# Kernel optimization log

Measured on AMD Instinct MI355X. Metric: run time of the kernel, lower is better.

## Reference

```python
import jax, jax.numpy as jnp
import numpy as np

N, F_IN, HID, HEADS, NEA, E, G = 50000, 32, 64, 2, 2, 800000, 50
SLOPE = 0.2  # leaky_relu negative_slope


def setup_inputs() -> dict:
    key = jax.random.key(0)
    ks = jax.random.split(key, 24)
    x = jax.random.normal(ks[0], (N, F_IN), jnp.float32)
    src = jax.random.randint(ks[1], (E,), 0, N, jnp.int32)
    off = jax.random.randint(ks[2], (E,), 1, N, jnp.int32)
    dst = ((src + off) % N).astype(jnp.int32)  # guaranteed no self loops
    edge_index = jnp.stack([src, dst])
    edge_attr = jax.random.uniform(ks[3], (E, NEA), jnp.float32, 0.5, 3.0)  # distances (reciprocal taken in fwd)
    batch = (jnp.arange(N) // (N // G)).astype(jnp.int32)
    interface_pos = jnp.arange(0, N, 5, dtype=jnp.int32)  # 200 interface nodes/graph

    def glorot(k, shape, fan_in, fan_out):
        s = jnp.sqrt(6.0 / (fan_in + fan_out))
        return jax.random.uniform(k, shape, jnp.float32, -s, s)

    HC = HEADS * HID
    W0 = glorot(ks[4], (F_IN, HC), F_IN, HC)
    attl0 = glorot(ks[5], (HEADS, HID), HID, HID)
    attr0 = glorot(ks[6], (HEADS, HID), HID, HID)
    W12 = glorot(ks[7], (2, HID, HC), HID, HC)
    attl12 = glorot(ks[8], (2, HEADS, HID), HID, HID)
    attr12 = glorot(ks[9], (2, HEADS, HID), HID, HID)
    eW = glorot(ks[10], (3, NEA, HC), NEA, HC)
    eb = jnp.zeros((3, HC), jnp.float32)
    bconv = jnp.zeros((3, HID), jnp.float32)
    gate_w = glorot(ks[11], (HID, 1), HID, 1)
    gate_b = jnp.zeros((1,), jnp.float32)
    lin1_w = glorot(ks[12], (4 * HID, 2 * HID), 4 * HID, 2 * HID)
    lin1_b = jnp.zeros((2 * HID,), jnp.float32)
    lin2_w = glorot(ks[13], (2 * HID, 1), 2 * HID, 1)
    lin2_b = jnp.zeros((1,), jnp.float32)
    return dict(x=x, edge_index=edge_index, edge_attr=edge_attr, batch=batch,
                interface_pos=interface_pos, graph_num=G,
                W0=W0, attl0=attl0, attr0=attr0, W12=W12, attl12=attl12, attr12=attr12,
                eW=eW, eb=eb, bconv=bconv, gate_w=gate_w, gate_b=gate_b,
                lin1_w=lin1_w, lin1_b=lin1_b, lin2_w=lin2_w, lin2_b=lin2_b)


def segment_softmax(e, seg, n):
    m = jax.ops.segment_max(e, seg, num_segments=n)
    ex = jnp.exp(e - m[seg])
    d = jax.ops.segment_sum(ex, seg, num_segments=n)
    return ex / (d[seg] + 1e-16)


def gate_conv(h, W, att_l, att_r, eW, eb, b, src, dst, ea):
    # GATEConv, concat=False, dropout in eval mode (identity)
    n = h.shape[0]
    H, C = att_l.shape
    xl = (h @ W).reshape(n, H, C)                      # lin_l == lin_r
    al = (xl * att_l).sum(-1)                          # [N,H]
    ar = (xl * att_r).sum(-1)
    e = jax.nn.leaky_relu(al[src] + ar[dst], SLOPE)    # [E+N,H]
    alpha = segment_softmax(e, dst, n)
    ee = (ea @ eW + eb).reshape(-1, H, C)              # edge embeddings
    msg = (xl[src] + ee) * alpha[..., None]
    out = jax.ops.segment_sum(msg, dst, num_segments=n)
    return out.mean(1) + b                             # mean over heads + bias


def reference(x, edge_index, edge_attr, batch, interface_pos, graph_num,
              W0, attl0, attr0, W12, attl12, attr12, eW, eb, bconv,
              gate_w, gate_b, lin1_w, lin1_b, lin2_w, lin2_b):
    n = x.shape[0]
    ar_n = jnp.arange(n, dtype=edge_index.dtype)
    src = jnp.concatenate([edge_index[0], ar_n])       # add self loops
    dst = jnp.concatenate([edge_index[1], ar_n])
    ea = jnp.concatenate([1.0 / edge_attr,
                          jnp.zeros((n, edge_attr.shape[1]), edge_attr.dtype)], 0)

    h = jnp.tanh(gate_conv(x, W0, attl0, attr0, eW[0], eb[0], bconv[0], src, dst, ea))
    xmax = h
    for l in range(2):  # num_layers - 1 structurally distinct weight slices
        h = jnp.tanh(gate_conv(h, W12[l], attl12[l], attr12[l],
                               eW[l + 1], eb[l + 1], bconv[l + 1], src, dst, ea))
        xmax = jnp.maximum(xmax, h)                    # JumpingKnowledge('max')

    xi = xmax[interface_pos]                           # [Ni, hidden]
    bi = batch[interface_pos]
    add = jax.ops.segment_sum(xi, bi, num_segments=graph_num)
    cnt = jax.ops.segment_sum(jnp.ones((xi.shape[0],), xi.dtype), bi, num_segments=graph_num)
    mean = add / jnp.maximum(cnt, 1.0)[:, None]
    gate = (xi @ gate_w + gate_b)[:, 0]                # global self-attention gate
    a = segment_softmax(gate, bi, graph_num)
    attp = jax.ops.segment_sum(a[:, None] * xi, bi, num_segments=graph_num)
    mx = jax.ops.segment_max(xi, bi, num_segments=graph_num)
    pooled = jnp.concatenate([add, mean, attp, mx], -1)  # [G, 4*hidden]
    z = jnp.tanh(pooled @ lin1_w + lin1_b)             # dropout eval = identity
    return z @ lin2_w + lin2_b                         # [G, 1]
```

## Files before the change

### kernel.cpp

```cpp
#include <hip/hip_runtime.h>
#include <hip/hip_bf16.h>
#include <hip/hip_fp16.h>
#include <math.h>

#define N_NODES 50000
#define FIN     32
#define HID     64
#define HC      128
#define NE      800000
#define NET     850000
#define NI      10000
#define NG      50
#define NPG     1000
#define NIPG    200
#define DMAX    64

#define EB512   ((NET + 511) / 512)
#define LBLK    (N_NODES / 16)

typedef _Float16 half8 __attribute__((ext_vector_type(8)));
typedef float float4v __attribute__((ext_vector_type(4)));

__device__ __forceinline__ float lrelu(float x) { return fmaxf(x, 0.2f * x); }

__device__ __forceinline__ float rlf(float v, int l) {
  return __int_as_float(__builtin_amdgcn_readlane(__float_as_int(v), l));
}
__device__ __forceinline__ int rli(int v, int l) {
  return __builtin_amdgcn_readlane(v, l);
}

template <int F>
__device__ __forceinline__ void lin8(
    int n0, const float* __restrict__ W,
    const float* __restrict__ attl, const float* __restrict__ attr,
    __half2* __restrict__ xl2h, float* __restrict__ al, float* __restrict__ ar,
    const _Float16* hA, _Float16* hC, float* redl, float* redr) {
  const int w = threadIdx.x >> 6, lane = threadIdx.x & 63;
  const int m = lane & 15, q = lane >> 4;

  half8 a0, a1;
#pragma unroll
  for (int j = 0; j < 8; j++) a0[j] = hA[m * F + q * 8 + j];
  if constexpr (F == 64) {
#pragma unroll
    for (int j = 0; j < 8; j++) a1[j] = hA[m * F + 32 + q * 8 + j];
  }

  const int colg = w * 16 + m;
  half8 b0;
#pragma unroll
  for (int j = 0; j < 8; j++) b0[j] = (_Float16)W[(q * 8 + j) * HC + colg];
  float4v z = {0.f, 0.f, 0.f, 0.f};
  float4v acc = __builtin_amdgcn_mfma_f32_16x16x32_f16(a0, b0, z, 0, 0, 0);
  if constexpr (F == 64) {
    half8 b1;
#pragma unroll
    for (int j = 0; j < 8; j++) b1[j] = (_Float16)W[(32 + q * 8 + j) * HC + colg];
    acc = __builtin_amdgcn_mfma_f32_16x16x32_f16(a1, b1, acc, 0, 0, 0);
  }
  const float atl = attl[colg], atr = attr[colg];
  float pl[4], pr[4];
#pragma unroll
  for (int reg = 0; reg < 4; reg++) {
    float val = acc[reg];
    hC[(q * 4 + reg) * 128 + colg] = (_Float16)val;
    pl[reg] = val * atl;
    pr[reg] = val * atr;
  }
#pragma unroll
  for (int off = 1; off < 16; off <<= 1) {
#pragma unroll
    for (int reg = 0; reg < 4; reg++) {
      pl[reg] += __shfl_xor(pl[reg], off, 64);
      pr[reg] += __shfl_xor(pr[reg], off, 64);
    }
  }
  if (m == 0) {
#pragma unroll
    for (int reg = 0; reg < 4; reg++) {
      redl[(q * 4 + reg) * 8 + w] = pl[reg];
      redr[(q * 4 + reg) * 8 + w] = pr[reg];
    }
  }
  __syncthreads();
  if (threadIdx.x < 32) {
    int node = threadIdx.x >> 1, head = threadIdx.x & 1;
    float sl = 0.f, sr = 0.f;
#pragma unroll
    for (int k = 0; k < 4; k++) {
      sl += redl[node * 8 + head * 4 + k];
      sr += redr[node * 8 + head * 4 + k];
    }
    al[(n0 + node) * 2 + head] = sl;
    ar[(n0 + node) * 2 + head] = sr;
  }
  for (int i = threadIdx.x; i < 16 * 64; i += 512) {
    int node = i >> 6, cc = i & 63;
    xl2h[(size_t)(n0 + node) * HID + cc] =
        __halves2half2(hC[node * 128 + cc], hC[node * 128 + 64 + cc]);
  }
}

__device__ __forceinline__ void agg_wave(
    int n0, const __half2* __restrict__ xl, const float* __restrict__ alp,
    const float2* __restrict__ ar2,
    const int* __restrict__ degarr, const int2* __restrict__ erec,
    const float* __restrict__ eW2, const float* __restrict__ eb1,
    const float* __restrict__ bconv1, float& outA, float& outB) {
  const int gid0 = n0 + ((threadIdx.x >> 6) << 1);
  const int lane = threadIdx.x & 63;
  const int l32 = lane & 31;
  const int half = lane >> 5;
  const int lane4 = lane << 2;
  const int gidH = gid0 + half;
  const int o0H = gidH * DMAX;
  const int degH = min(degarr[gidH], DMAX);
  const float2 arvH = ar2[gidH];
  const char* xbase = (const char*)xl;
  const char* albase = (const char*)alp;

  const int degA = rli(degH, 0);
  const int degB = rli(degH, 32);
  const int degmax = max(degA, degB);

  float aA0 = 0.f, aA1 = 0.f, bA0 = 0.f, bA1 = 0.f;
  float aB0 = 0.f, aB1 = 0.f, bB0 = 0.f, bB1 = 0.f;
  float ld0 = 0.f, ld1 = 0.f, lex0 = 0.f, ley0 = 0.f, lex1 = 0.f, ley1 = 0.f;

  for (int base = 0; base < degmax; base += 32) {
    int j = base + l32;
    int soff = 0; float p0 = 0.f, p1 = 0.f;
    if (j < degH) {
      int2 r = erec[o0H + j];
      soff = r.x;
      float2 eaf = __half22float2(*(__half2*)&r.y);
      float2 alv = *(const float2*)(albase + (soff >> 5));
      p0 = __expf(lrelu(alv.x + arvH.x));
      p1 = __expf(lrelu(alv.y + arvH.y));
      ld0 += p0; ld1 += p1;
      lex0 += p0 * eaf.x; ley0 += p0 * eaf.y;
      lex1 += p1 * eaf.x; ley1 += p1 * eaf.y;
    }
    int lenA = min(32, degA - base); lenA = max(lenA, 0);
    int lenB = min(32, degB - base); lenB = max(lenB, 0);
    int lenA4 = (lenA + 3) & ~3;
    int lenB4 = (lenB + 3) & ~3;
    int len = max(lenA4, lenB4);
    for (int j2 = 0; j2 < len; j2 += 4) {
      if (j2 < lenA4) {
        float2 x0 = __half22float2(*(const __half2*)(xbase + rli(soff, j2)     + lane4));
        float2 x1 = __half22float2(*(const __half2*)(xbase + rli(soff, j2 + 1) + lane4));
        float2 x2 = __half22float2(*(const __half2*)(xbase + rli(soff, j2 + 2) + lane4));
        float2 x3 = __half22float2(*(const __half2*)(xbase + rli(soff, j2 + 3) + lane4));
        aA0 += rlf(p0, j2)     * x0.x; aA1 += rlf(p1, j2)     * x0.y;
        bA0 += rlf(p0, j2 + 1) * x1.x; bA1 += rlf(p1, j2 + 1) * x1.y;
        aA0 += rlf(p0, j2 + 2) * x2.x; aA1 += rlf(p1, j2 + 2) * x2.y;
        bA0 += rlf(p0, j2 + 3) * x3.x; bA1 += rlf(p1, j2 + 3) * x3.y;
      }
      if (j2 < lenB4) {
        float2 x4 = __half22float2(*(const __half2*)(xbase + rli(soff, 32 + j2)     + lane4));
        float2 x5 = __half22float2(*(const __half2*)(xbase + rli(soff, 32 + j2 + 1) + lane4));
        float2 x6 = __half22float2(*(const __half2*)(xbase + rli(soff, 32 + j2 + 2) + lane4));
        float2 x7 = __half22float2(*(const __half2*)(xbase + rli(soff, 32 + j2 + 3) + lane4));
        aB0 += rlf(p0, 32 + j2)     * x4.x; aB1 += rlf(p1, 32 + j2)     * x4.y;
        bB0 += rlf(p0, 32 + j2 + 1) * x5.x; bB1 += rlf(p1, 32 + j2 + 1) * x5.y;
        aB0 += rlf(p0, 32 + j2 + 2) * x6.x; aB1 += rlf(p1, 32 + j2 + 2) * x6.y;
        bB0 += rlf(p0, 32 + j2 + 3) * x7.x; bB1 += rlf(p1, 32 + j2 + 3) * x7.y;
      }
    }
  }
  float accA0 = aA0 + bA0, accA1 = aA1 + bA1;
  float accB0 = aB0 + bB0, accB1 = aB1 + bB1;
#pragma unroll
  for (int off = 16; off; off >>= 1) {
    ld0  += __shfl_xor(ld0, off, 64);
    ld1  += __shfl_xor(ld1, off, 64);
    lex0 += __shfl_xor(lex0, off, 64);
    ley0 += __shfl_xor(ley0, off, 64);
    lex1 += __shfl_xor(lex1, off, 64);
    ley1 += __shfl_xor(ley1, off, 64);
  }
  float ld0A  = __shfl(ld0,  l32, 64), ld0B  = __shfl(ld0,  32 + l32, 64);
  float ld1A  = __shfl(ld1,  l32, 64), ld1B  = __shfl(ld1,  32 + l32, 64);
  float lex0A = __shfl(lex0, l32, 64), lex0B = __shfl(lex0, 32 + l32, 64);
  float ley0A = __shfl(ley0, l32, 64), ley0B = __shfl(ley0, 32 + l32, 64);
  float lex1A = __shfl(lex1, l32, 64), lex1B = __shfl(lex1, 32 + l32, 64);
  float ley1A = __shfl(ley1, l32, 64), ley1B = __shfl(ley1, 32 + l32, 64);

  const float w00 = eW2[lane],      w01 = eW2[HC + lane],      b0v = eb1[lane];
  const float w10 = eW2[64 + lane], w11 = eW2[HC + 64 + lane], b1v = eb1[64 + lane];
  const float bc = bconv1[lane];

  float tA0 = accA0 + w00 * lex0A + w01 * ley0A + b0v * ld0A;
  float tA1 = accA1 + w10 * lex1A + w11 * ley1A + b1v * ld1A;
  float tB0 = accB0 + w00 * lex0B + w01 * ley0B + b0v * ld0B;
  float tB1 = accB1 + w10 * lex1B + w11 * ley1B + b1v * ld1B;
  outA = tanhf(0.5f * (tA0 / (ld0A + 1e-16f) + tA1 / (ld1A + 1e-16f)) + bc);
  outB = tanhf(0.5f * (tB0 / (ld0B + 1e-16f) + tB1 / (ld1B + 1e-16f)) + bc);
}

__global__ __launch_bounds__(512) void k_build_lin0(
    const int* __restrict__ ei, const float* __restrict__ eattr,
    int* __restrict__ deg, int2* __restrict__ erec,
    const float* __restrict__ x, const float* __restrict__ W0,
    const float* __restrict__ attl0, const float* __restrict__ attr0,
    __half2* __restrict__ xl2h, float* __restrict__ al, float* __restrict__ ar) {
  __shared__ _Float16 hA[16 * FIN];
  __shared__ _Float16 hC[16 * 128];
  __shared__ float redl[128], redr[128];
  int b = blockIdx.x;
  if (b < EB512) {
    int e = b * 512 + threadIdx.x;
    if (e < NET) {
      int s, d; float ex, ey;
      if (e < NE) {
        s = ei[e]; d = ei[NE + e];
        float2 ea = ((const float2*)eattr)[e];
        ex = 1.0f / ea.x; ey = 1.0f / ea.y;
      } else {
        s = d = e - NE; ex = 0.f; ey = 0.f;
      }
      int r = atomicAdd(&deg[d], 1);
      if (r < DMAX) {
        __half2 ea2 = __floats2half2_rn(ex, ey);
        erec[d * DMAX + r] = make_int2(s << 8, *(int*)&ea2);
      }
    }
    return;
  }
  const int n0 = (b - EB512) * 16;
  for (int i = threadIdx.x; i < 16 * FIN; i += 512)
    hA[i] = (_Float16)x[(size_t)n0 * FIN + i];
  __syncthreads();
  lin8<FIN>(n0, W0, attl0, attr0, xl2h, al, ar, hA, hC, redl, redr);
}

__global__ __launch_bounds__(512) void k_agg_lin(
    const __half2* __restrict__ xl_in, const float* __restrict__ al_in,
    const float2* __restrict__ ar2,
    const int* __restrict__ degarr, const int2* __restrict__ erec,
    const float* __restrict__ eW2, const float* __restrict__ eb1,
    const float* __restrict__ bconv1, float* __restrict__ hout,
    const float* __restrict__ Wn, const float* __restrict__ attln,
    const float* __restrict__ attrn, __half2* __restrict__ xl_out,
    float* __restrict__ al_out, float* __restrict__ ar_out) {
  __shared__ _Float16 hA[16 * HID];
  __shared__ _Float16 hC[16 * 128];
  __shared__ float redl[128], redr[128];
  const int n0 = blockIdx.x * 16;
  float rA, rB;
  agg_wave(n0, xl_in, al_in, ar2, degarr, erec, eW2, eb1, bconv1, rA, rB);
  const int w = threadIdx.x >> 6, lane = threadIdx.x & 63;
  hout[(size_t)(n0 + 2 * w) * HID + lane] = rA;
  hout[(size_t)(n0 + 2 * w + 1) * HID + lane] = rB;
  hA[(2 * w) * HID + lane] = (_Float16)rA;
  hA[(2 * w + 1) * HID + lane] = (_Float16)rB;
  __syncthreads();
  lin8<HID>(n0, Wn, attln, attrn, xl_out, al_out, ar_out, hA, hC, redl, redr);
}

__global__ __launch_bounds__(512) void k_agg_xi(
    const __half2* __restrict__ xl_in, const float* __restrict__ al_in,
    const float2* __restrict__ ar2,
    const int* __restrict__ degarr, const int2* __restrict__ erec,
    const float* __restrict__ eW2, const float* __restrict__ eb1,
    const float* __restrict__ bconv1, const float* __restrict__ h0,
    const float* __restrict__ h1, const float* __restrict__ gate_w,
    const float* __restrict__ gate_b, float* __restrict__ xi,
    float* __restrict__ gexp) {
  const int n0 = blockIdx.x * 16;
  float rA, rB;
  agg_wave(n0, xl_in, al_in, ar2, degarr, erec, eW2, eb1, bconv1, rA, rB);
  const int w = threadIdx.x >> 6, lane = threadIdx.x & 63;
  const int nA = n0 + 2 * w, nB = nA + 1;
  const float gwv = gate_w[lane];
  const float gbv = gate_b[0];
  if (nA % 5 == 0) {
    float v = fmaxf(fmaxf(h0[(size_t)nA * HID + lane], h1[(size_t)nA * HID + lane]), rA);
    int idx = nA / 5;
    xi[(size_t)idx * HID + lane] = v;
    float gv = v * gwv;
#pragma unroll
    for (int off = 32; off; off >>= 1) gv += __shfl_xor(gv, off, 64);
    if (lane == 0) gexp[idx] = __expf(gv + gbv);
  }
  if (nB % 5 == 0) {
    float v = fmaxf(fmaxf(h0[(size_t)nB * HID + lane], h1[(size_t)nB * HID + lane]), rB);
    int idx = nB / 5;
    xi[(size_t)idx * HID + lane] = v;
    float gv = v * gwv;
#pragma unroll
    for (int off = 32; off; off >>= 1) gv += __shfl_xor(gv, off, 64);
    if (lane == 0) gexp[idx] = __expf(gv + gbv);
  }
}

__global__ __launch_bounds__(256) void k_final(
    const float* __restrict__ xi, const float* __restrict__ gexp,
    const float* __restrict__ lin1_w, const float* __restrict__ lin1_b,
    const float* __restrict__ lin2_w, const float* __restrict__ lin2_b,
    float* __restrict__ out) {
  __shared__ float red[4][3 * HID + 1];
  __shared__ float pooled[4 * HID];
  __shared__ float zred[2 * HID];
  const int g = blockIdx.x, t = threadIdx.x;
  const int w = t >> 6, lane = t & 63;

  float padd = 0.f, pmax = -1e30f, pattp = 0.f, paden = 0.f;
  for (int i = w; i < NIPG; i += 4) {
    int idx = g * NIPG + i;
    float v = xi[(size_t)idx * HID + lane];
    float e = gexp[idx];
    padd += v;
    pmax = fmaxf(pmax, v);
    pattp += e * v;
    paden += e;
  }
  red[w][lane] = padd;
  red[w][HID + lane] = pmax;
  red[w][2 * HID + lane] = pattp;
  if (lane == 0) red[w][3 * HID] = paden;
  __syncthreads();
  if (t < HID) {
    float a  = red[0][t] + red[1][t] + red[2][t] + red[3][t];
    float mx = fmaxf(fmaxf(red[0][HID + t], red[1][HID + t]),
                     fmaxf(red[2][HID + t], red[3][HID + t]));
    float ap = red[0][2 * HID + t] + red[1][2 * HID + t] +
               red[2][2 * HID + t] + red[3][2 * HID + t];
    float ad = red[0][3 * HID] + red[1][3 * HID] + red[2][3 * HID] + red[3][3 * HID];
    pooled[t]           = a;
    pooled[HID + t]     = a * (1.0f / NIPG);
    pooled[2 * HID + t] = ap / (ad + 1e-16f);
    pooled[3 * HID + t] = mx;
  }
  __syncthreads();
  if (t < 2 * HID) {
    float z = lin1_b[t];
    for (int k = 0; k < 4 * HID; k++) z += pooled[k] * lin1_w[k * (2 * HID) + t];
    z = tanhf(z);
    zred[t] = z * lin2_w[t];
  }
  __syncthreads();
  if (t == 0) {
    float s = 0.f;
    for (int k = 0; k < 2 * HID; k++) s += zred[k];
    out[g] = s + lin2_b[0];
  }
}

extern "C" void kernel_launch(void* const* d_in, const int* in_sizes, int n_in,
                              void* d_out, int out_size, void* d_ws, size_t ws_size,
                              hipStream_t stream) {
  const float* x      = (const float*)d_in[0];
  const int*   ei     = (const int*)d_in[1];
  const float* eattr  = (const float*)d_in[2];
  const float* W0     = (const float*)d_in[6];
  const float* attl0  = (const float*)d_in[7];
  const float* attr0  = (const float*)d_in[8];
  const float* W12    = (const float*)d_in[9];
  const float* attl12 = (const float*)d_in[10];
  const float* attr12 = (const float*)d_in[11];
  const float* eW     = (const float*)d_in[12];
  const float* eb     = (const float*)d_in[13];
  const float* bconv  = (const float*)d_in[14];
  const float* gate_w = (const float*)d_in[15];
  const float* gate_b = (const float*)d_in[16];
  const float* lin1_w = (const float*)d_in[17];
  const float* lin1_b = (const float*)d_in[18];
  const float* lin2_w = (const float*)d_in[19];
  const float* lin2_b = (const float*)d_in[20];
  float* out = (float*)d_out;

  char* ws = (char*)d_ws;
  size_t off = 0;
  auto alloc = [&](size_t elems) {
    void* p = ws + off;
    off += ((elems * 4 + 15) / 16) * 16;
    return p;
  };
  int*      deg    = (int*)alloc(N_NODES);
  size_t zbytes = off;
  int2*    erec   = (int2*)alloc((size_t)N_NODES * DMAX * 2);
  __half2* xl2hA  = (__half2*)alloc((size_t)N_NODES * HID);
  __half2* xl2hB  = (__half2*)alloc((size_t)N_NODES * HID);
  float*   alA    = (float*)alloc((size_t)N_NODES * 2);
  float*   alB    = (float*)alloc((size_t)N_NODES * 2);
  float*   arr    = (float*)alloc((size_t)N_NODES * 2);
  float*   h0     = (float*)alloc((size_t)N_NODES * HID);
  float*   h1     = (float*)alloc((size_t)N_NODES * HID);
  float*   xi     = (float*)alloc((size_t)NI * HID);
  float*   gexp   = (float*)alloc(NI);
  (void)ws_size; (void)in_sizes; (void)n_in; (void)out_size;

  hipMemsetAsync(d_ws, 0, zbytes, stream);

  k_build_lin0<<<EB512 + LBLK, 512, 0, stream>>>(ei, eattr, deg, erec,
                                                 x, W0, attl0, attr0, xl2hA, alA, arr);
  k_agg_lin<<<LBLK, 512, 0, stream>>>(xl2hA, alA, (const float2*)arr, deg, erec,
                                      eW, eb, bconv, h0,
                                      W12, attl12, attr12, xl2hB, alB, arr);
  k_agg_lin<<<LBLK, 512, 0, stream>>>(xl2hB, alB, (const float2*)arr, deg, erec,
                                      eW + 2 * HC, eb + HC, bconv + HID, h1,
                                      W12 + (size_t)HID * HC, attl12 + HC, attr12 + HC,
                                      xl2hA, alA, arr);
  k_agg_xi<<<LBLK, 512, 0, stream>>>(xl2hA, alA, (const float2*)arr, deg, erec,
                                     eW + 4 * HC, eb + 2 * HC, bconv + 2 * HID,
                                     h0, h1, gate_w, gate_b, xi, gexp);
  k_final<<<NG, 256, 0, stream>>>(xi, gexp, lin1_w, lin1_b, lin2_w, lin2_b, out);
}
```

Measured before the change: 330.0 us.

## Split fused aggregate+linear kernels into separate build, linear and aggregate kernels

Unfuses the graph build from the layer-0 linear and splits each aggregate+linear kernel into a standalone aggregation kernel and a standalone MFMA linear kernel, using 256-thread blocks. The linear now round-trips hidden states through global memory in fp32 (h0/h1 re-read) instead of passing them through shared memory. The aim appears to be higher occupancy and better latency hiding in the gather-heavy aggregation by shrinking blocks. In exchange it adds three kernel launches and extra global traffic per layer.

```diff
diff --git a/kernel.cpp b/kernel.cpp
--- a/kernel.cpp
+++ b/kernel.cpp
@@ -15,8 +15,8 @@
 #define NIPG    200
 #define DMAX    64
 
-#define EB512   ((NET + 511) / 512)
 #define LBLK    (N_NODES / 16)
+#define ABLK    (N_NODES / 8)
 
 typedef _Float16 half8 __attribute__((ext_vector_type(8)));
 typedef float float4v __attribute__((ext_vector_type(4)));
@@ -30,14 +30,40 @@
   return __builtin_amdgcn_readlane(v, l);
 }
 
+__global__ void k_build(const int* __restrict__ ei, const float* __restrict__ eattr,
+                        int* __restrict__ deg, int2* __restrict__ erec) {
+  int e = blockIdx.x * blockDim.x + threadIdx.x;
+  if (e >= NET) return;
+  int s, d; float ex, ey;
+  if (e < NE) {
+    s = ei[e]; d = ei[NE + e];
+    float2 ea = ((const float2*)eattr)[e];
+    ex = 1.0f / ea.x; ey = 1.0f / ea.y;
+  } else {
+    s = d = e - NE; ex = 0.f; ey = 0.f;
+  }
+  int r = atomicAdd(&deg[d], 1);
+  if (r < DMAX) {
+    __half2 ea2 = __floats2half2_rn(ex, ey);
+    erec[d * DMAX + r] = make_int2(s << 8, *(int*)&ea2);
+  }
+}
+
 template <int F>
-__device__ __forceinline__ void lin8(
-    int n0, const float* __restrict__ W,
+__global__ __launch_bounds__(256) void k_linear_mfma(
+    const float* __restrict__ h, const float* __restrict__ W,
     const float* __restrict__ attl, const float* __restrict__ attr,
-    __half2* __restrict__ xl2h, float* __restrict__ al, float* __restrict__ ar,
-    const _Float16* hA, _Float16* hC, float* redl, float* redr) {
+    __half2* __restrict__ xl2h, float* __restrict__ al, float* __restrict__ ar) {
+  __shared__ _Float16 hA[16 * F];
+  __shared__ _Float16 hC[16 * 128];
+  __shared__ float redl[16 * 4], redr[16 * 4];
   const int w = threadIdx.x >> 6, lane = threadIdx.x & 63;
   const int m = lane & 15, q = lane >> 4;
+  const int n0 = blockIdx.x * 16;
+
+  for (int i = threadIdx.x; i < 16 * F; i += 256)
+    hA[i] = (_Float16)h[(size_t)n0 * F + i];
+  __syncthreads();
 
   half8 a0, a1;
 #pragma unroll
@@ -47,26 +73,31 @@
     for (int j = 0; j < 8; j++) a1[j] = hA[m * F + 32 + q * 8 + j];
   }
 
-  const int colg = w * 16 + m;
-  half8 b0;
-#pragma unroll
-  for (int j = 0; j < 8; j++) b0[j] = (_Float16)W[(q * 8 + j) * HC + colg];
-  float4v z = {0.f, 0.f, 0.f, 0.f};
-  float4v acc = __builtin_amdgcn_mfma_f32_16x16x32_f16(a0, b0, z, 0, 0, 0);
-  if constexpr (F == 64) {
-    half8 b1;
-#pragma unroll
-    for (int j = 0; j < 8; j++) b1[j] = (_Float16)W[(32 + q * 8 + j) * HC + colg];
-    acc = __builtin_amdgcn_mfma_f32_16x16x32_f16(a1, b1, acc, 0, 0, 0);
-  }
-  const float atl = attl[colg], atr = attr[colg];
-  float pl[4], pr[4];
-#pragma unroll
-  for (int reg = 0; reg < 4; reg++) {
-    float val = acc[reg];
-    hC[(q * 4 + reg) * 128 + colg] = (_Float16)val;
-    pl[reg] = val * atl;
-    pr[reg] = val * atr;
+  const int c0 = w * 32;
+  float4v acc[2];
+  float pl[4] = {0.f, 0.f, 0.f, 0.f}, pr[4] = {0.f, 0.f, 0.f, 0.f};
+#pragma unroll
+  for (int t = 0; t < 2; t++) {
+    const int colg = c0 + t * 16 + m;
+    half8 b0;
+#pragma unroll
+    for (int j = 0; j < 8; j++) b0[j] = (_Float16)W[(q * 8 + j) * HC + colg];
+    float4v z = {0.f, 0.f, 0.f, 0.f};
+    acc[t] = __builtin_amdgcn_mfma_f32_16x16x32_f16(a0, b0, z, 0, 0, 0);
+    if constexpr (F == 64) {
+      half8 b1;
+#pragma unroll
+      for (int j = 0; j < 8; j++) b1[j] = (_Float16)W[(32 + q * 8 + j) * HC + colg];
+      acc[t] = __builtin_amdgcn_mfma_f32_16x16x32_f16(a1, b1, acc[t], 0, 0, 0);
+    }
+    const float atl = attl[colg], atr = attr[colg];
+#pragma unroll
+    for (int reg = 0; reg < 4; reg++) {
+      float val = acc[t][reg];
+      hC[(q * 4 + reg) * 128 + colg] = (_Float16)val;
+      pl[reg] += val * atl;
+      pr[reg] += val * atr;
+    }
   }
 #pragma unroll
   for (int off = 1; off < 16; off <<= 1) {
@@ -79,23 +110,17 @@
   if (m == 0) {
 #pragma unroll
     for (int reg = 0; reg < 4; reg++) {
-      redl[(q * 4 + reg) * 8 + w] = pl[reg];
-      redr[(q * 4 + reg) * 8 + w] = pr[reg];
+      redl[(q * 4 + reg) * 4 + w] = pl[reg];
+      redr[(q * 4 + reg) * 4 + w] = pr[reg];
     }
   }
   __syncthreads();
   if (threadIdx.x < 32) {
     int node = threadIdx.x >> 1, head = threadIdx.x & 1;
-    float sl = 0.f, sr = 0.f;
-#pragma unroll
-    for (int k = 0; k < 4; k++) {
-      sl += redl[node * 8 + head * 4 + k];
-      sr += redr[node * 8 + head * 4 + k];
-    }
-    al[(n0 + node) * 2 + head] = sl;
-    ar[(n0 + node) * 2 + head] = sr;
-  }
-  for (int i = threadIdx.x; i < 16 * 64; i += 512) {
+    al[(n0 + node) * 2 + head] = redl[node * 4 + head * 2] + redl[node * 4 + head * 2 + 1];
+    ar[(n0 + node) * 2 + head] = redr[node * 4 + head * 2] + redr[node * 4 + head * 2 + 1];
+  }
+  for (int i = threadIdx.x; i < 16 * 64; i += 256) {
     int node = i >> 6, cc = i & 63;
     xl2h[(size_t)(n0 + node) * HID + cc] =
         __halves2half2(hC[node * 128 + cc], hC[node * 128 + 64 + cc]);
@@ -200,80 +225,35 @@
   outB = tanhf(0.5f * (tB0 / (ld0B + 1e-16f) + tB1 / (ld1B + 1e-16f)) + bc);
 }
 
-__global__ __launch_bounds__(512) void k_build_lin0(
-    const int* __restrict__ ei, const float* __restrict__ eattr,
-    int* __restrict__ deg, int2* __restrict__ erec,
-    const float* __restrict__ x, const float* __restrict__ W0,
-    const float* __restrict__ attl0, const float* __restrict__ attr0,
-    __half2* __restrict__ xl2h, float* __restrict__ al, float* __restrict__ ar) {
-  __shared__ _Float16 hA[16 * FIN];
-  __shared__ _Float16 hC[16 * 128];
-  __shared__ float redl[128], redr[128];
-  int b = blockIdx.x;
-  if (b < EB512) {
-    int e = b * 512 + threadIdx.x;
-    if (e < NET) {
-      int s, d; float ex, ey;
-      if (e < NE) {
-        s = ei[e]; d = ei[NE + e];
-        float2 ea = ((const float2*)eattr)[e];
-        ex = 1.0f / ea.x; ey = 1.0f / ea.y;
-      } else {
-        s = d = e - NE; ex = 0.f; ey = 0.f;
-      }
-      int r = atomicAdd(&deg[d], 1);
-      if (r < DMAX) {
-        __half2 ea2 = __floats2half2_rn(ex, ey);
-        erec[d * DMAX + r] = make_int2(s << 8, *(int*)&ea2);
-      }
-    }
-    return;
-  }
-  const int n0 = (b - EB512) * 16;
-  for (int i = threadIdx.x; i < 16 * FIN; i += 512)
-    hA[i] = (_Float16)x[(size_t)n0 * FIN + i];
-  __syncthreads();
-  lin8<FIN>(n0, W0, attl0, attr0, xl2h, al, ar, hA, hC, redl, redr);
-}
-
-__global__ __launch_bounds__(512) void k_agg_lin(
+__global__ __launch_bounds__(256) void k_aggregate(
     const __half2* __restrict__ xl_in, const float* __restrict__ al_in,
-    const float2* __restrict__ ar2,
-    const int* __restrict__ degarr, const int2* __restrict__ erec,
-    const float* __restrict__ eW2, const float* __restrict__ eb1,
-    const float* __restrict__ bconv1, float* __restrict__ hout,
-    const float* __restrict__ Wn, const float* __restrict__ attln,
-    const float* __restrict__ attrn, __half2* __restrict__ xl_out,
-    float* __restrict__ al_out, float* __restrict__ ar_out) {
-  __shared__ _Float16 hA[16 * HID];
-  __shared__ _Float16 hC[16 * 128];
-  __shared__ float redl[128], redr[128];
-  const int n0 = blockIdx.x * 16;
+    const float2* __restrict__ ar2, const int* __restrict__ degarr,
+    const int2* __restrict__ erec, const float* __restrict__ eW2,
+    const float* __restrict__ eb1, const float* __restrict__ bconv1,
+    float* __restrict__ hout) {
+  const int n0 = blockIdx.x * 8;
   float rA, rB;
   agg_wave(n0, xl_in, al_in, ar2, degarr, erec, eW2, eb1, bconv1, rA, rB);
-  const int w = threadIdx.x >> 6, lane = threadIdx.x & 63;
-  hout[(size_t)(n0 + 2 * w) * HID + lane] = rA;
-  hout[(size_t)(n0 + 2 * w + 1) * HID + lane] = rB;
-  hA[(2 * w) * HID + lane] = (_Float16)rA;
-  hA[(2 * w + 1) * HID + lane] = (_Float16)rB;
-  __syncthreads();
-  lin8<HID>(n0, Wn, attln, attrn, xl_out, al_out, ar_out, hA, hC, redl, redr);
-}
-
-__global__ __launch_bounds__(512) void k_agg_xi(
+  const int gid0 = n0 + ((threadIdx.x >> 6) << 1);
+  const int lane = threadIdx.x & 63;
+  hout[(size_t)gid0 * HID + lane] = rA;
+  hout[(size_t)(gid0 + 1) * HID + lane] = rB;
+}
+
+__global__ __launch_bounds__(256) void k_agg_xi(
     const __half2* __restrict__ xl_in, const float* __restrict__ al_in,
-    const float2* __restrict__ ar2,
-    const int* __restrict__ degarr, const int2* __restrict__ erec,
-    const float* __restrict__ eW2, const float* __restrict__ eb1,
-    const float* __restrict__ bconv1, const float* __restrict__ h0,
-    const float* __restrict__ h1, const float* __restrict__ gate_w,
-    const float* __restrict__ gate_b, float* __restrict__ xi,
-    float* __restrict__ gexp) {
-  const int n0 = blockIdx.x * 16;
+    const float2* __restrict__ ar2, const int* __restrict__ degarr,
+    const int2* __restrict__ erec, const float* __restrict__ eW2,
+    const float* __restrict__ eb1, const float* __restrict__ bconv1,
+    const float* __restrict__ h0, const float* __restrict__ h1,
+    const float* __restrict__ gate_w, const float* __restrict__ gate_b,
+    float* __restrict__ xi, float* __restrict__ gexp) {
+  const int n0 = blockIdx.x * 8;
   float rA, rB;
   agg_wave(n0, xl_in, al_in, ar2, degarr, erec, eW2, eb1, bconv1, rA, rB);
-  const int w = threadIdx.x >> 6, lane = threadIdx.x & 63;
-  const int nA = n0 + 2 * w, nB = nA + 1;
+  const int gid0 = n0 + ((threadIdx.x >> 6) << 1);
+  const int lane = threadIdx.x & 63;
+  const int nA = gid0, nB = gid0 + 1;
   const float gwv = gate_w[lane];
   const float gbv = gate_b[0];
   if (nA % 5 == 0) {
@@ -395,16 +375,16 @@
 
   hipMemsetAsync(d_ws, 0, zbytes, stream);
 
-  k_build_lin0<<<EB512 + LBLK, 512, 0, stream>>>(ei, eattr, deg, erec,
-                                                 x, W0, attl0, attr0, xl2hA, alA, arr);
-  k_agg_lin<<<LBLK, 512, 0, stream>>>(xl2hA, alA, (const float2*)arr, deg, erec,
-                                      eW, eb, bconv, h0,
-                                      W12, attl12, attr12, xl2hB, alB, arr);
-  k_agg_lin<<<LBLK, 512, 0, stream>>>(xl2hB, alB, (const float2*)arr, deg, erec,
-                                      eW + 2 * HC, eb + HC, bconv + HID, h1,
-                                      W12 + (size_t)HID * HC, attl12 + HC, attr12 + HC,
-                                      xl2hA, alA, arr);
-  k_agg_xi<<<LBLK, 512, 0, stream>>>(xl2hA, alA, (const float2*)arr, deg, erec,
+  k_build<<<(NET + 255) / 256, 256, 0, stream>>>(ei, eattr, deg, erec);
+  k_linear_mfma<FIN><<<LBLK, 256, 0, stream>>>(x, W0, attl0, attr0, xl2hA, alA, arr);
+  k_aggregate<<<ABLK, 256, 0, stream>>>(xl2hA, alA, (const float2*)arr, deg, erec,
+                                        eW, eb, bconv, h0);
+  k_linear_mfma<HID><<<LBLK, 256, 0, stream>>>(h0, W12, attl12, attr12, xl2hB, alB, arr);
+  k_aggregate<<<ABLK, 256, 0, stream>>>(xl2hB, alB, (const float2*)arr, deg, erec,
+                                        eW + 2 * HC, eb + HC, bconv + HID, h1);
+  k_linear_mfma<HID><<<LBLK, 256, 0, stream>>>(h1, W12 + (size_t)HID * HC,
+                                               attl12 + HC, attr12 + HC, xl2hA, alA, arr);
+  k_agg_xi<<<ABLK, 256, 0, stream>>>(xl2hA, alA, (const float2*)arr, deg, erec,
                                      eW + 4 * HC, eb + 2 * HC, bconv + 2 * HID,
                                      h0, h1, gate_w, gate_b, xi, gexp);
   k_final<<<NG, 256, 0, stream>>>(xi, gexp, lin1_w, lin1_b, lin2_w, lin2_b, out);
```

Result: no change. 330.1 us, median of 2 (+0.0%).
